# Performance work log

Hardware: AMD Instinct MI355X
Metric: run time of the kernel (lower is better)

The kernel has to match this reference:

```python
import jax, jax.numpy as jnp
import numpy as np

EPS = 1e-8

def _cosine_sim(a, b):
    # a: [B,Nq,D], b: [B,Np,D] -> [B,Nq,Np]
    an = a / (jnp.linalg.norm(a, axis=-1, keepdims=True) + EPS)
    bn = b / (jnp.linalg.norm(b, axis=-1, keepdims=True) + EPS)
    return jnp.einsum('bqd,bpd->bqp', an, bn)

def _sq_dist(a, b):
    # squared euclidean pairwise distance: [B,Nq,Np]
    d = (jnp.sum(a * a, -1)[:, :, None] + jnp.sum(b * b, -1)[:, None, :]
         - 2.0 * jnp.einsum('bqd,bpd->bqp', a, b))
    return jnp.maximum(d, 0.0)

def setup_inputs() -> dict:
    key = jax.random.key(0)
    ks = jax.random.split(key, 6)
    B, N, D, H = 8, 2048, 256, 16
    return {
        'f1': jax.random.normal(ks[0], (B, N, D), jnp.float32),
        'f2': jax.random.normal(ks[1], (B, N, D), jnp.float32),
        'p': jax.random.normal(ks[2], (B, N, 3), jnp.float32),
        'q': jax.random.normal(ks[3], (B, N, 3), jnp.float32),
        'W1': jax.random.normal(ks[4], (H, 2), jnp.float32) * 0.5,
        'b1': jnp.zeros((H,), jnp.float32),
        'W2': jax.random.normal(ks[5], (1, H), jnp.float32) * 0.5,
        'b2': jnp.zeros((1,), jnp.float32),
        'similar_num': 8,
    }

def reference(f1, f2, p, q, W1, b1, W2, b2, similar_num):
    B, Nq, _ = q.shape
    Np = p.shape[1]
    # pairwise similarities
    w1 = _cosine_sim(f2, f1)            # [B,Nq,Np] feature cosine sim
    w2 = -_sq_dist(q, p)                # [B,Nq,Np] negative coord distance
    # similar_net: pointwise MLP over channel dim (2 -> H -> 1)
    w_in = jnp.stack([w1.reshape(B, -1), w2.reshape(B, -1)], axis=1)  # [B,2,L]
    h = jax.nn.relu(jnp.einsum('bcl,hc->bhl', w_in, W1) + b1[None, :, None])
    w = (jnp.einsum('bhl,oh->bol', h, W2) + b2[None, :, None]).reshape(B, Nq, Np)
    # get_weighted_similarity: topk + softmax-weighted pooling + max pooling
    vals, idx = jax.lax.top_k(w, similar_num)          # [B,Nq,k] (sorted desc, as torch.topk)
    ws = jax.nn.softmax(vals, axis=-1)                 # softmax over gathered scores
    feat = jax.vmap(lambda z, i: z[i])(f1, idx)        # [B,Nq,k,D] gather
    feat_max = jnp.max(feat, axis=2)                   # [B,Nq,D]
    feat_w = jnp.einsum('bqk,bqkd->bqd', ws, feat)     # [B,Nq,D]
    f = jnp.concatenate([feat_w, feat_max], axis=-1)   # [B,Nq,2D]
    return f, idx, w
```

## Files before the change

### kernel.cpp

```cpp
#include <hip/hip_runtime.h>
#include <math.h>

constexpr int B_ = 8;
constexpr int N_ = 2048;
constexpr int D_ = 256;
constexpr int H_ = 16;
constexpr int K_ = 8;
constexpr int POOL = 64;
constexpr int PSEL = 24;

constexpr int BM = 128;
constexpr int BK = 32;

typedef _Float16 f16x8 __attribute__((ext_vector_type(8)));
typedef float    f32x4 __attribute__((ext_vector_type(4)));
typedef float    f32x2 __attribute__((ext_vector_type(2)));

typedef __attribute__((address_space(3))) unsigned int       lds_u32_t;
typedef __attribute__((address_space(1))) const unsigned int glb_u32_t;

__device__ __forceinline__ void g2l16(const void* g, void* l) {
    __builtin_amdgcn_global_load_lds((glb_u32_t*)g, (lds_u32_t*)l, 16, 0, 0);
}

__device__ __forceinline__ unsigned ford(float f) {
    unsigned u = __float_as_uint(f);
    return (u & 0x80000000u) ? ~u : (u | 0x80000000u);
}
__device__ __forceinline__ float unford(unsigned t) {
    return (t & 0x80000000u) ? __uint_as_float(t & 0x7FFFFFFFu)
                             : __uint_as_float(~t);
}

__device__ __forceinline__ unsigned pk16(_Float16 a, _Float16 b) {
    unsigned short ua = __builtin_bit_cast(unsigned short, a);
    unsigned short ub = __builtin_bit_cast(unsigned short, b);
    return (unsigned)ua | ((unsigned)ub << 16);
}

__device__ inline void split4_f16(float4 v, float s, uint2& hi, uint2& lo) {
    float a = v.x * s, b = v.y * s, c = v.z * s, d = v.w * s;
    _Float16 ha = (_Float16)a, hb = (_Float16)b;
    _Float16 hc = (_Float16)c, hd = (_Float16)d;
    _Float16 la = (_Float16)(a - (float)ha), lb = (_Float16)(b - (float)hb);
    _Float16 lc = (_Float16)(c - (float)hc), ld = (_Float16)(d - (float)hd);
    hi.x = pk16(ha, hb); hi.y = pk16(hc, hd);
    lo.x = pk16(la, lb); lo.y = pk16(lc, ld);
}

__global__ __launch_bounds__(256)
void prep_kernel(const float* __restrict__ f1, const float* __restrict__ f2,
                 const float* __restrict__ pcoord, const float* __restrict__ qcoord,
                 unsigned short* __restrict__ s1h, unsigned short* __restrict__ s1l,
                 unsigned short* __restrict__ s2h,
                 unsigned short* __restrict__ qaug, unsigned short* __restrict__ paug,
                 double* __restrict__ dinv1) {
    int gid  = blockIdx.x * blockDim.x + threadIdx.x;
    int wave = gid >> 6;
    int lane = gid & 63;
    if (wave >= 2 * B_ * N_) return;
    bool is1 = wave < B_ * N_;
    int r = is1 ? wave : wave - B_ * N_;

    const float* src = (is1 ? f1 : f2) + (size_t)r * D_;
    float4 v = *(const float4*)(src + lane * 4);
    float ss = v.x * v.x + v.y * v.y + v.z * v.z + v.w * v.w;
#pragma unroll
    for (int off = 32; off > 0; off >>= 1) ss += __shfl_xor(ss, off, 64);
    float inv = 1.0f / (sqrtf(ss) + 1e-8f);

    uint2 hi, lo;
    split4_f16(v, inv, hi, lo);

    int panel = r >> 7, rloc = r & 127;
    int s     = lane >> 1;
    int chunk = s >> 2;
    int sl    = (s & 3) ^ ((rloc >> 1) & 3);
    int half  = lane & 1;
    size_t idx = ((size_t)(panel * 8 + chunk) << 12)
               + (size_t)rloc * 32 + sl * 8 + half * 4;
    if (is1) {
        *(uint2*)&s1h[idx] = hi;
        *(uint2*)&s1l[idx] = lo;
        double dss = (double)v.x * v.x + (double)v.y * v.y
                   + (double)v.z * v.z + (double)v.w * v.w;
#pragma unroll
        for (int off = 32; off > 0; off >>= 1) dss += __shfl_xor(dss, off, 64);
        if (lane == 0) dinv1[r] = 1.0 / (sqrt(dss) + 1e-8);
    } else {
        *(uint2*)&s2h[idx] = hi;
    }

    if (lane == 0) {
        const float* cp = (is1 ? pcoord : qcoord) + (size_t)r * 3;
        float x = cp[0], y = cp[1], z = cp[2];
        const float s2 = 1.41421356237309515f;
        _Float16 xh = (_Float16)(s2 * x), yh = (_Float16)(s2 * y), zh = (_Float16)(s2 * z);
        _Float16 xl = (_Float16)(s2 * x - (float)xh);
        _Float16 yl = (_Float16)(s2 * y - (float)yh);
        _Float16 zl = (_Float16)(s2 * z - (float)zh);
        float nn = x * x + y * y + z * z;
        _Float16 nh = (_Float16)nn, nl = (_Float16)(nn - (float)nh);
        _Float16 one = (_Float16)1.0f;
        _Float16 mnh = -nh, mnl = -nl;
        unsigned short h[32];
#pragma unroll
        for (int i = 0; i < 32; i++) h[i] = 0;
#define US_(v) __builtin_bit_cast(unsigned short, v)
        if (is1) {
            h[0] = US_(xh); h[1] = US_(yh); h[2] = US_(zh);
            h[3] = US_(xh); h[4] = US_(yh); h[5] = US_(zh);
            h[6] = US_(xl); h[7] = US_(yl); h[8] = US_(zl);
            h[9] = US_(one); h[10] = US_(one);
            h[11] = US_(mnh); h[12] = US_(mnl);
        } else {
            h[0] = US_(xh); h[1] = US_(yh); h[2] = US_(zh);
            h[3] = US_(xl); h[4] = US_(yl); h[5] = US_(zl);
            h[6] = US_(xh); h[7] = US_(yh); h[8] = US_(zh);
            h[9] = US_(mnh); h[10] = US_(mnl);
            h[11] = US_(one); h[12] = US_(one);
        }
#undef US_
        unsigned short* dst = (is1 ? paug : qaug) + (size_t)r * 32;
#pragma unroll
        for (int i = 0; i < 4; i++) ((uint4*)dst)[i] = ((const uint4*)h)[i];
    }
}

__global__ __launch_bounds__(256, 3)
void gemm_mlp_kernel(const unsigned short* __restrict__ aH0,
                     const unsigned short* __restrict__ bH0,
                     const unsigned short* __restrict__ bL0,
                     const unsigned short* __restrict__ qaug,
                     const unsigned short* __restrict__ paug,
                     const float* __restrict__ pW1, const float* __restrict__ pb1,
                     const float* __restrict__ pW2, const float* __restrict__ pb2,
                     float* __restrict__ w_out) {
    __shared__ unsigned short ldsbuf[2 * 3 * 4096];

    int tid = threadIdx.x;
    int l  = blockIdx.x + (blockIdx.y << 4);
    int ls = ((l & 7) << 5) | (l >> 3);
    int pBase = (ls & 15) * BM;
    int qBase = (ls >> 4) * BM;
    int b = blockIdx.z;

    int lane = tid & 63;
    int wv   = tid >> 6;
    int wq = (wv >> 1) * 64;
    int wp = (wv & 1) * 64;
    int fr = lane & 15;
    int kg = lane >> 4;

    const int Apanel8 = ((b * N_ + qBase) >> 7) * 8;
    const int Bpanel8 = ((b * N_ + pBase) >> 7) * 8;

    char* ldsB = (char*)&ldsbuf[0];
    const int wlo = (wv << 11) + (lane << 4);
    const int wdo = (wv << 11);
    const int cw  = (kg ^ ((fr >> 1) & 3)) << 4;

    f32x4 acc[4][4] = {};

#define STAGE(buf, c)                                                          \
    {                                                                          \
        const char* aH = (const char*)aH0 + ((size_t)(Apanel8 + (c)) << 13);   \
        const char* bH = (const char*)bH0 + ((size_t)(Bpanel8 + (c)) << 13);   \
        const char* bL = (const char*)bL0 + ((size_t)(Bpanel8 + (c)) << 13);   \
        char* dst = ldsB + (buf) * 24576;                                      \
        _Pragma("unroll")                                                      \
        for (int i = 0; i < 2; i++) {                                          \
            int o = i << 10;                                                   \
            g2l16(aH + wlo + o, dst + 0     + wdo + o);                        \
            g2l16(bH + wlo + o, dst + 8192  + wdo + o);                        \
            g2l16(bL + wlo + o, dst + 16384 + wdo + o);                        \
        }                                                                      \
    }

    STAGE(0, 0);
    __syncthreads();

#pragma unroll
    for (int c = 0; c < 8; c++) {
        if (c < 7) STAGE((c + 1) & 1, c + 1);

        char* base = ldsB + (c & 1) * 24576;
        f16x8 ah[4], bh[4], bl[4];
#pragma unroll
        for (int t = 0; t < 4; t++) {
            int ra = (wq + t * 16 + fr) * 64;
            int rb = (wp + t * 16 + fr) * 64;
            ah[t] = *(const f16x8*)(base + 0     + ra + cw);
            bh[t] = *(const f16x8*)(base + 8192  + rb + cw);
            bl[t] = *(const f16x8*)(base + 16384 + rb + cw);
        }
#pragma unroll
        for (int qt = 0; qt < 4; qt++) {
#pragma unroll
            for (int pt = 0; pt < 4; pt++) {
                acc[qt][pt] = __builtin_amdgcn_mfma_f32_16x16x32_f16(
                    ah[qt], bh[pt], acc[qt][pt], 0, 0, 0);
                acc[qt][pt] = __builtin_amdgcn_mfma_f32_16x16x32_f16(
                    ah[qt], bl[pt], acc[qt][pt], 0, 0, 0);
            }
        }
        __syncthreads();
    }
#undef STAGE

    f32x2 Wap[8], Wbp[8], Bbp[8], Wop[8];
#pragma unroll
    for (int hp = 0; hp < 8; hp++) {
        Wap[hp] = (f32x2){pW1[4 * hp],     pW1[4 * hp + 2]};
        Wbp[hp] = (f32x2){pW1[4 * hp + 1], pW1[4 * hp + 3]};
        Bbp[hp] = (f32x2){pb1[2 * hp],     pb1[2 * hp + 1]};
        Wop[hp] = (f32x2){pW2[2 * hp],     pW2[2 * hp + 1]};
    }
    float b2v = pb2[0];

    const unsigned short* qa_base = qaug + ((size_t)(b * N_ + qBase + wq) << 5) + kg * 8;
    const unsigned short* pa_base = paug + ((size_t)(b * N_ + pBase + wp) << 5) + kg * 8;

#pragma unroll
    for (int qt = 0; qt < 4; qt++) {
        f16x8 aaug = *(const f16x8*)(qa_base + ((qt * 16 + fr) << 5));
        int rowb = qBase + wq + qt * 16 + kg * 4;
#pragma unroll
        for (int pt = 0; pt < 4; pt++) {
            f16x8 baug = *(const f16x8*)(pa_base + ((pt * 16 + fr) << 5));
            f32x4 sacc = __builtin_amdgcn_mfma_f32_16x16x32_f16(
                aaug, baug, (f32x4){0.f, 0.f, 0.f, 0.f}, 0, 0, 0);
            f32x4 cval = acc[qt][pt];
            int col = pBase + wp + pt * 16 + fr;
#pragma unroll
            for (int r = 0; r < 4; r++) {
                float w1 = cval[r];
                float w2 = fminf(sacc[r], 0.f);
                f32x2 w1p = {w1, w1}, w2p = {w2, w2};
                f32x2 o = {b2v, 0.f};
#pragma unroll
                for (int hp = 0; hp < 8; hp++) {
                    f32x2 t = __builtin_elementwise_fma(w2p, Wbp[hp], Bbp[hp]);
                    t = __builtin_elementwise_fma(w1p, Wap[hp], t);
                    t = __builtin_elementwise_max(t, (f32x2){0.f, 0.f});
                    o = __builtin_elementwise_fma(t, Wop[hp], o);
                }
                w_out[((size_t)(b * N_ + rowb + r)) * N_ + col] = o.x + o.y;
            }
        }
    }
}

__global__ __launch_bounds__(256)
void topk_kernel(const float* __restrict__ w, const float* __restrict__ f1,
                 const float* __restrict__ f2,
                 const float* __restrict__ pc, const float* __restrict__ qc,
                 const float* __restrict__ pW1, const float* __restrict__ pb1,
                 const float* __restrict__ pW2, const float* __restrict__ pb2,
                 const double* __restrict__ dinv1,
                 float* __restrict__ f_out, float* __restrict__ idx_out) {
    __shared__ int    s_cand[4][POOL];
    __shared__ double s_val[4][POOL];
    __shared__ int    s_idx[4][POOL];
    __shared__ double s_rv[4][K_];
    __shared__ int    s_ri[4][K_];

    int tid  = threadIdx.x;
    int wix  = tid >> 6;
    int lane = tid & 63;
    int row  = blockIdx.x * 4 + wix;
    int b    = row >> 11;
    const float* wrow = w + (size_t)row * N_;

    float4 v4s[8];
    float mymax = -INFINITY;
#pragma unroll
    for (int j = 0; j < 8; j++) {
        v4s[j] = *(const float4*)(wrow + lane * 4 + j * 256);
        mymax = fmaxf(mymax,
                 fmaxf(fmaxf(v4s[j].x, v4s[j].y), fmaxf(v4s[j].z, v4s[j].w)));
    }

    unsigned mk = ford(mymax);
    unsigned T = 0;
    for (int bit = 31; bit >= 0; --bit) {
        unsigned c = T | (1u << bit);
        if (__popcll(__ballot(mk >= c)) >= PSEL) T = c;
    }
    float Tf = unford(T);

    unsigned long long below = (1ull << lane) - 1ull;
    int total = 0;
#pragma unroll
    for (int j = 0; j < 8; j++) {
        float vv[4] = {v4s[j].x, v4s[j].y, v4s[j].z, v4s[j].w};
#pragma unroll
        for (int c = 0; c < 4; c++) {
            bool in = vv[c] >= Tf;
            unsigned long long m = __ballot(in);
            if (in) {
                int pos = total + __popcll(m & below);
                if (pos < POOL) s_cand[wix][pos] = lane * 4 + j * 256 + c;
            }
            total += __popcll(m);
        }
    }
    int ncand = total < POOL ? total : POOL;
    asm volatile("s_waitcnt lgkmcnt(0)" ::: "memory");

    int sl = lane & 7;
    int gr = lane >> 3;
    const float* f2r = f2 + (size_t)row * D_ + sl * 32;
    float4 a4[8];
#pragma unroll
    for (int t = 0; t < 8; t++) a4[t] = *(const float4*)(f2r + t * 4);

    double daa = 0.0;
#pragma unroll
    for (int t = 0; t < 8; t++) {
        daa += (double)a4[t].x * (double)a4[t].x;
        daa += (double)a4[t].y * (double)a4[t].y;
        daa += (double)a4[t].z * (double)a4[t].z;
        daa += (double)a4[t].w * (double)a4[t].w;
    }
#pragma unroll
    for (int off = 1; off < 8; off <<= 1) daa += __shfl_xor(daa, off, 64);
    double inv_a = 1.0 / (sqrt(daa) + 1e-8);

    double mydab = 0.0;
    int myci = 0;
    int NR = (ncand + 7) >> 3;
    for (int r = 0; r < NR; r++) {
        int k = 8 * r + gr;
        int cj = (k < ncand) ? s_cand[wix][k] : 0;
        const float* f1r = f1 + ((size_t)(b * N_ + cj)) * D_ + sl * 32;
        double sA = 0.0;
#pragma unroll
        for (int t = 0; t < 8; t++) {
            float4 b4 = *(const float4*)(f1r + t * 4);
            sA += (double)a4[t].x * (double)b4.x;
            sA += (double)a4[t].y * (double)b4.y;
            sA += (double)a4[t].z * (double)b4.z;
            sA += (double)a4[t].w * (double)b4.w;
        }
#pragma unroll
        for (int off = 1; off < 8; off <<= 1) sA += __shfl_xor(sA, off, 64);
        if (sl == r) { mydab = sA; myci = cj; }
    }

    int myk = 8 * sl + gr;
    double ex = -INFINITY;
    int    ei = 0x7fffffff;
    if (myk < ncand) {
        ei = myci;
        double w1d = mydab * inv_a * dinv1[b * N_ + myci];
        const float* qp = qc + (size_t)row * 3;
        double qx = qp[0], qy = qp[1], qz = qp[2];
        const float* pp = pc + ((size_t)(b * N_ + myci)) * 3;
        double px = pp[0], py = pp[1], pz = pp[2];
        double d2 = (qx * qx + qy * qy + qz * qz) + (px * px + py * py + pz * pz)
                  - 2.0 * (qx * px + qy * py + qz * pz);
        double w2d = -fmax(d2, 0.0);
        double out = (double)pb2[0];
#pragma unroll
        for (int h = 0; h < H_; h++) {
            double t = (double)pW1[2 * h] * w1d + (double)pW1[2 * h + 1] * w2d
                     + (double)pb1[h];
            out += (double)pW2[h] * fmax(t, 0.0);
        }
        ex = out;
    }

    s_val[wix][myk] = ex;
    s_idx[wix][myk] = ei;
    asm volatile("s_waitcnt lgkmcnt(0)" ::: "memory");
    {
        int rank = 0;
#pragma unroll
        for (int j = 0; j < POOL; j++) {
            double vj = s_val[wix][j];
            int    ij = s_idx[wix][j];
            rank += (vj > ex || (vj == ex && ij < ei)) ? 1 : 0;
        }
        if (rank < K_) { s_rv[wix][rank] = ex; s_ri[wix][rank] = ei; }
    }
    asm volatile("s_waitcnt lgkmcnt(0)" ::: "memory");

    double outv[K_];
    int    outi[K_];
#pragma unroll
    for (int r = 0; r < K_; r++) { outv[r] = s_rv[wix][r]; outi[r] = s_ri[wix][r]; }

    float m = (float)outv[0];
    float e[K_], s = 0.f;
#pragma unroll
    for (int r = 0; r < K_; r++) { e[r] = expf((float)outv[r] - m); s += e[r]; }
    float inv_s = 1.f / s;

    const float* f1b = f1 + ((size_t)b * N_) * D_;
    size_t obase = (size_t)row * (2 * D_);
#pragma unroll
    for (int jd = 0; jd < D_ / 64; jd++) {
        int d = lane + 64 * jd;
        float accv = 0.f, mx = -INFINITY;
#pragma unroll
        for (int r = 0; r < K_; r++) {
            float x = f1b[(size_t)outi[r] * D_ + d];
            accv += (e[r] * inv_s) * x;
            mx = fmaxf(mx, x);
        }
        f_out[obase + d]      = accv;
        f_out[obase + D_ + d] = mx;
    }
    if (lane == 0) {
#pragma unroll
        for (int r = 0; r < K_; r++) idx_out[(size_t)row * K_ + r] = (float)outi[r];
    }
}

extern "C" void kernel_launch(void* const* d_in, const int* in_sizes, int n_in,
                              void* d_out, int out_size, void* d_ws, size_t ws_size,
                              hipStream_t stream) {
    const float* f1 = (const float*)d_in[0];
    const float* f2 = (const float*)d_in[1];
    const float* pc = (const float*)d_in[2];
    const float* qc = (const float*)d_in[3];
    const float* W1 = (const float*)d_in[4];
    const float* b1 = (const float*)d_in[5];
    const float* W2 = (const float*)d_in[6];
    const float* b2 = (const float*)d_in[7];

    float* out     = (float*)d_out;
    float* f_out   = out;
    float* idx_out = f_out + (size_t)B_ * N_ * 2 * D_;
    float* w_out   = idx_out + (size_t)B_ * N_ * K_;

    unsigned short* s1h  = (unsigned short*)f_out;
    unsigned short* s1l  = s1h + (size_t)B_ * N_ * D_;
    unsigned short* s2h  = s1l + (size_t)B_ * N_ * D_;
    unsigned short* qaug = s2h + (size_t)B_ * N_ * D_;
    unsigned short* paug = qaug + (size_t)B_ * N_ * 32;

    double* dinv1 = (double*)d_ws;

    prep_kernel<<<(2 * B_ * N_) / 4, 256, 0, stream>>>(f1, f2, pc, qc,
                                                       s1h, s1l, s2h,
                                                       qaug, paug, dinv1);

    dim3 g2(N_ / BM, N_ / BM, B_);
    gemm_mlp_kernel<<<g2, 256, 0, stream>>>(s2h, s1h, s1l, qaug, paug,
                                            W1, b1, W2, b2, w_out);

    topk_kernel<<<(B_ * N_) / 4, 256, 0, stream>>>(w_out, f1, f2, pc, qc,
                                                   W1, b1, W2, b2, dinv1,
                                                   f_out, idx_out);
}
```

Before: 379.0 us.

## Precompute f2 inverse norms, shrink candidate pool, and split dot-product accumulators

The prep kernel now also writes f2 inverse norms in double to workspace when there is room, so the top-k kernel can skip recomputing them. PSEL drops from 24 to 16, which changes how the candidate threshold is picked and likely shrinks the refinement pool. The rescoring dot product is split across four double accumulators for more instruction-level parallelism, and the rank loop runs only over real candidates. The smaller PSEL may let true top-k entries fall outside the pool, and the new path depends on workspace size.

```diff
diff --git a/kernel.cpp b/kernel.cpp
--- a/kernel.cpp
+++ b/kernel.cpp
@@ -7,7 +7,7 @@
 constexpr int H_ = 16;
 constexpr int K_ = 8;
 constexpr int POOL = 64;
-constexpr int PSEL = 24;
+constexpr int PSEL = 16;
 
 constexpr int BM = 128;
 constexpr int BK = 32;
@@ -54,7 +54,7 @@
                  unsigned short* __restrict__ s1h, unsigned short* __restrict__ s1l,
                  unsigned short* __restrict__ s2h,
                  unsigned short* __restrict__ qaug, unsigned short* __restrict__ paug,
-                 double* __restrict__ dinv1) {
+                 double* __restrict__ dinv1, double* __restrict__ dinv2) {
     int gid  = blockIdx.x * blockDim.x + threadIdx.x;
     int wave = gid >> 6;
     int lane = gid & 63;
@@ -79,14 +79,22 @@
     int half  = lane & 1;
     size_t idx = ((size_t)(panel * 8 + chunk) << 12)
                + (size_t)rloc * 32 + sl * 8 + half * 4;
+
+    bool wantd = is1 || (dinv2 != nullptr);
+    if (wantd) {
+        double dss = (double)v.x * v.x + (double)v.y * v.y
+                   + (double)v.z * v.z + (double)v.w * v.w;
+#pragma unroll
+        for (int off = 32; off > 0; off >>= 1) dss += __shfl_xor(dss, off, 64);
+        if (lane == 0) {
+            double dv = 1.0 / (sqrt(dss) + 1e-8);
+            if (is1) dinv1[r] = dv; else dinv2[r] = dv;
+        }
+    }
+
     if (is1) {
         *(uint2*)&s1h[idx] = hi;
         *(uint2*)&s1l[idx] = lo;
-        double dss = (double)v.x * v.x + (double)v.y * v.y
-                   + (double)v.z * v.z + (double)v.w * v.w;
-#pragma unroll
-        for (int off = 32; off > 0; off >>= 1) dss += __shfl_xor(dss, off, 64);
-        if (lane == 0) dinv1[r] = 1.0 / (sqrt(dss) + 1e-8);
     } else {
         *(uint2*)&s2h[idx] = hi;
     }
@@ -257,7 +265,7 @@
                  const float* __restrict__ pc, const float* __restrict__ qc,
                  const float* __restrict__ pW1, const float* __restrict__ pb1,
                  const float* __restrict__ pW2, const float* __restrict__ pb2,
-                 const double* __restrict__ dinv1,
+                 const double* __restrict__ dinv1, const double* __restrict__ dinv2,
                  float* __restrict__ f_out, float* __restrict__ idx_out) {
     __shared__ int    s_cand[4][POOL];
     __shared__ double s_val[4][POOL];
@@ -310,39 +318,53 @@
 
     int sl = lane & 7;
     int gr = lane >> 3;
-    const float* f2r = f2 + (size_t)row * D_ + sl * 32;
+    const float* f2r = f2 + ((size_t)row << 8) + sl * 32;
     float4 a4[8];
 #pragma unroll
     for (int t = 0; t < 8; t++) a4[t] = *(const float4*)(f2r + t * 4);
 
-    double daa = 0.0;
-#pragma unroll
-    for (int t = 0; t < 8; t++) {
-        daa += (double)a4[t].x * (double)a4[t].x;
-        daa += (double)a4[t].y * (double)a4[t].y;
-        daa += (double)a4[t].z * (double)a4[t].z;
-        daa += (double)a4[t].w * (double)a4[t].w;
-    }
-#pragma unroll
-    for (int off = 1; off < 8; off <<= 1) daa += __shfl_xor(daa, off, 64);
-    double inv_a = 1.0 / (sqrt(daa) + 1e-8);
-
+    double inv_a;
+    if (dinv2) {
+        inv_a = dinv2[row];
+    } else {
+        double daa = 0.0;
+#pragma unroll
+        for (int t = 0; t < 8; t++) {
+            daa += (double)a4[t].x * (double)a4[t].x;
+            daa += (double)a4[t].y * (double)a4[t].y;
+            daa += (double)a4[t].z * (double)a4[t].z;
+            daa += (double)a4[t].w * (double)a4[t].w;
+        }
+#pragma unroll
+        for (int off = 1; off < 8; off <<= 1) daa += __shfl_xor(daa, off, 64);
+        inv_a = 1.0 / (sqrt(daa) + 1e-8);
+    }
+
+    const float* f1bb = f1 + ((size_t)(b * N_) << 8);
     double mydab = 0.0;
     int myci = 0;
     int NR = (ncand + 7) >> 3;
     for (int r = 0; r < NR; r++) {
         int k = 8 * r + gr;
         int cj = (k < ncand) ? s_cand[wix][k] : 0;
-        const float* f1r = f1 + ((size_t)(b * N_ + cj)) * D_ + sl * 32;
-        double sA = 0.0;
-#pragma unroll
-        for (int t = 0; t < 8; t++) {
-            float4 b4 = *(const float4*)(f1r + t * 4);
-            sA += (double)a4[t].x * (double)b4.x;
-            sA += (double)a4[t].y * (double)b4.y;
-            sA += (double)a4[t].z * (double)b4.z;
-            sA += (double)a4[t].w * (double)b4.w;
-        }
+        const float* f1r = f1bb + ((unsigned)(cj << 8)) + sl * 32;
+        double ps0 = 0.0, ps1 = 0.0, ps2 = 0.0, ps3 = 0.0;
+#pragma unroll
+        for (int t = 0; t < 8; t += 4) {
+            float4 b0 = *(const float4*)(f1r + t * 4);
+            float4 b1 = *(const float4*)(f1r + t * 4 + 4);
+            float4 b2 = *(const float4*)(f1r + t * 4 + 8);
+            float4 b3 = *(const float4*)(f1r + t * 4 + 12);
+            ps0 += (double)a4[t].x * b0.x + (double)a4[t].y * b0.y
+                 + (double)a4[t].z * b0.z + (double)a4[t].w * b0.w;
+            ps1 += (double)a4[t+1].x * b1.x + (double)a4[t+1].y * b1.y
+                 + (double)a4[t+1].z * b1.z + (double)a4[t+1].w * b1.w;
+            ps2 += (double)a4[t+2].x * b2.x + (double)a4[t+2].y * b2.y
+                 + (double)a4[t+2].z * b2.z + (double)a4[t+2].w * b2.w;
+            ps3 += (double)a4[t+3].x * b3.x + (double)a4[t+3].y * b3.y
+                 + (double)a4[t+3].z * b3.z + (double)a4[t+3].w * b3.w;
+        }
+        double sA = (ps0 + ps1) + (ps2 + ps3);
 #pragma unroll
         for (int off = 1; off < 8; off <<= 1) sA += __shfl_xor(sA, off, 64);
         if (sl == r) { mydab = sA; myci = cj; }
@@ -376,13 +398,12 @@
     asm volatile("s_waitcnt lgkmcnt(0)" ::: "memory");
     {
         int rank = 0;
-#pragma unroll
-        for (int j = 0; j < POOL; j++) {
+        for (int j = 0; j < ncand; j++) {
             double vj = s_val[wix][j];
             int    ij = s_idx[wix][j];
             rank += (vj > ex || (vj == ex && ij < ei)) ? 1 : 0;
         }
-        if (rank < K_) { s_rv[wix][rank] = ex; s_ri[wix][rank] = ei; }
+        if (rank < K_ && myk < ncand) { s_rv[wix][rank] = ex; s_ri[wix][rank] = ei; }
     }
     asm volatile("s_waitcnt lgkmcnt(0)" ::: "memory");
 
@@ -442,16 +463,18 @@
     unsigned short* paug = qaug + (size_t)B_ * N_ * 32;
 
     double* dinv1 = (double*)d_ws;
+    double* dinv2 = (ws_size >= (size_t)2 * B_ * N_ * sizeof(double))
+                  ? dinv1 + (size_t)B_ * N_ : nullptr;
 
     prep_kernel<<<(2 * B_ * N_) / 4, 256, 0, stream>>>(f1, f2, pc, qc,
                                                        s1h, s1l, s2h,
-                                                       qaug, paug, dinv1);
+                                                       qaug, paug, dinv1, dinv2);
 
     dim3 g2(N_ / BM, N_ / BM, B_);
     gemm_mlp_kernel<<<g2, 256, 0, stream>>>(s2h, s1h, s1l, qaug, paug,
                                             W1, b1, W2, b2, w_out);
 
     topk_kernel<<<(B_ * N_) / 4, 256, 0, stream>>>(w_out, f1, f2, pc, qc,
-                                                   W1, b1, W2, b2, dinv1,
+                                                   W1, b1, W2, b2, dinv1, dinv2,
                                                    f_out, idx_out);
 }
```

Measured after the change: 343.9 us. -9.2%, faster.
